# Optimization experiments

Hardware: AMD Instinct MI355X
Metric: run time of the kernel (lower is better)

The kernel has to match this reference:

```python
import jax, jax.numpy as jnp
import numpy as np

N = 50000
E = 400000


def _cheb_norm(edge_index, dtype):
    # PyG ChebConv norm (normalization='sym', lambda_max=2.0):
    # remove self loops, L_hat = -D^{-1/2} A D^{-1/2} on off-diagonal edges.
    src, dst = edge_index[0], edge_index[1]
    mask = (src != dst).astype(dtype)
    deg = jax.ops.segment_sum(mask, src, num_segments=N)
    dinv = jnp.where(deg > 0, jax.lax.rsqrt(jnp.where(deg > 0, deg, 1.0)), 0.0)
    w = -dinv[src] * dinv[dst] * mask  # [E]
    return src, dst, w


def _cheb_conv(x, src, dst, w, W0, W1, b):
    # out = T0(x) W0 + T1(x) W1 + b, T0 = x, T1 = L_hat x
    tx1 = jax.ops.segment_sum(w[:, None] * x[src], dst, num_segments=N)
    return x @ W0 + tx1 @ W1 + b


def setup_inputs() -> dict:
    key = jax.random.key(0)
    ks = jax.random.split(key, 12)
    s = 0.05
    inp = {
        "x": jax.random.normal(ks[0], (N, 128), dtype=jnp.float32),
        "edge_index": jax.random.randint(ks[1], (2, E), 0, N, dtype=jnp.int64),
        "W1_0": jax.random.normal(ks[2], (128, 256), dtype=jnp.float32) * s,
        "W1_1": jax.random.normal(ks[3], (128, 256), dtype=jnp.float32) * s,
        "b1": jnp.zeros((256,), dtype=jnp.float32),
        "W2_0": jax.random.normal(ks[4], (256, 256), dtype=jnp.float32) * s,
        "W2_1": jax.random.normal(ks[5], (256, 256), dtype=jnp.float32) * s,
        "b2": jnp.zeros((256,), dtype=jnp.float32),
        "W3_0": jax.random.normal(ks[6], (256, 256), dtype=jnp.float32) * s,
        "W3_1": jax.random.normal(ks[7], (256, 256), dtype=jnp.float32) * s,
        "b3": jnp.zeros((256,), dtype=jnp.float32),
    }
    return inp


def reference(x, edge_index, W1_0, W1_1, b1, W2_0, W2_1, b2, W3_0, W3_1, b3):
    # Eval mode: F.dropout with training=False is identity, so dropout is omitted.
    src, dst, w = _cheb_norm(edge_index, x.dtype)
    h = jax.nn.relu(_cheb_conv(x, src, dst, w, W1_0, W1_1, b1))
    h = jax.nn.relu(_cheb_conv(h, src, dst, w, W2_0, W2_1, b2))
    h = _cheb_conv(h, src, dst, w, W3_0, W3_1, b3)
    return h
```

## Files before the change

kernel.cpp:

```cpp
#include <hip/hip_runtime.h>
#include <hip/hip_bf16.h>


typedef __attribute__((ext_vector_type(8))) short bf16x8;
typedef __attribute__((ext_vector_type(4))) float f32x4;

__device__ __forceinline__ float bf2f(unsigned int lo16) {
    unsigned int t = lo16 << 16;
    return __builtin_bit_cast(float, t);
}
__device__ __forceinline__ unsigned short f2bf(float f) {
    unsigned int u = __builtin_bit_cast(unsigned int, f);
    unsigned int r = (u + 0x7fffu + ((u >> 16) & 1u)) >> 16;
    return (unsigned short)r;
}

struct PrepParams {
    const int* src;
    const int* dst;
    int* deg;
    int* cnt;
    int* rank;
    int E;
    const float* x;
    unsigned short* xb;
    int gE;
    int gC;
    const float* W[6];
    unsigned short* WT[6];
    int K[6];
};

__global__ __launch_bounds__(256) void prep_kernel(PrepParams p) {
    __shared__ float t[32][33];
    int b = blockIdx.x;
    int tid = threadIdx.x;
    if (b < p.gE) {
        int e = b * 256 + tid;
        if (e < p.E) {
            int s = p.src[e], d = p.dst[e];
            if (s != d) atomicAdd(&p.deg[s], 1);
            p.rank[e] = atomicAdd(&p.cnt[d], 1);
        }
        return;
    }
    b -= p.gE;
    if (b < p.gC) {
        long long i = (long long)b * 256 + tid;
        float4 v = reinterpret_cast<const float4*>(p.x)[i];
        ushort4 o;
        o.x = f2bf(v.x); o.y = f2bf(v.y); o.z = f2bf(v.z); o.w = f2bf(v.w);
        reinterpret_cast<ushort4*>(p.xb)[i] = o;
        return;
    }
    b -= p.gC;
    int m = b >> 6;
    int rem = b & 63;
    int K = p.K[m];
    int kb = (rem & 7) * 32, nb = (rem >> 3) * 32;
    if (kb >= K) return;
    const float* W = p.W[m];
    unsigned short* WT = p.WT[m];
    int lx = tid & 31, ly = tid >> 5;
    #pragma unroll
    for (int i = 0; i < 32; i += 8)
        t[ly + i][lx] = W[(size_t)(kb + ly + i) * 256 + nb + lx];
    __syncthreads();
    #pragma unroll
    for (int i = 0; i < 32; i += 8)
        WT[(size_t)(nb + ly + i) * K + kb + lx] = f2bf(t[lx][ly + i]);
}

__global__ __launch_bounds__(256) void scan_partial_dinv(const int* __restrict__ cnt,
                                                         int* __restrict__ part,
                                                         int* __restrict__ deg, int N) {
    __shared__ int lds[256];
    int tid = threadIdx.x;
    int base = blockIdx.x * 1024 + tid * 4;
    int s = 0;
    #pragma unroll
    for (int i = 0; i < 4; ++i) {
        if (base + i < N) {
            s += cnt[base + i];
            int d = deg[base + i];
            float dv = (d > 0) ? rsqrtf((float)d) : 0.0f;
            reinterpret_cast<float*>(deg)[base + i] = dv;
        }
    }
    lds[tid] = s;
    __syncthreads();
    for (int off = 128; off > 0; off >>= 1) {
        if (tid < off) lds[tid] += lds[tid + off];
        __syncthreads();
    }
    if (tid == 0) part[blockIdx.x] = lds[0];
}

__global__ __launch_bounds__(256) void scan_chunk(const int* __restrict__ cnt,
                                                  const int* __restrict__ part,
                                                  int* __restrict__ rowptr, int N, int NB) {
    __shared__ int lds[256];
    __shared__ int blockOff;
    int tid = threadIdx.x;
    if (tid < 64) {
        int v = (tid < NB) ? part[tid] : 0;
        int inc = v;
        #pragma unroll
        for (int off = 1; off < 64; off <<= 1) {
            int t = __shfl_up(inc, off, 64);
            if (tid >= off) inc += t;
        }
        if (tid == (int)blockIdx.x) blockOff = inc - v;
        if (blockIdx.x == 0 && tid == NB - 1) rowptr[N] = inc;
    }
    __syncthreads();
    int base = blockIdx.x * 1024 + tid * 4;
    int c[4];
    #pragma unroll
    for (int i = 0; i < 4; ++i) c[i] = (base + i < N) ? cnt[base + i] : 0;
    int ts = c[0] + c[1] + c[2] + c[3];
    lds[tid] = ts;
    __syncthreads();
    for (int off = 1; off < 256; off <<= 1) {
        int v = (tid >= off) ? lds[tid - off] : 0;
        __syncthreads();
        lds[tid] += v;
        __syncthreads();
    }
    int o = blockOff + lds[tid] - ts;
    #pragma unroll
    for (int i = 0; i < 4; ++i) {
        if (base + i < N) rowptr[base + i] = o;
        o += c[i];
    }
}

__global__ __launch_bounds__(256) void fill_kernel(const int* __restrict__ src,
                                                   const int* __restrict__ dst,
                                                   const int* __restrict__ rank,
                                                   const float* __restrict__ dinv,
                                                   const int* __restrict__ rowptr,
                                                   int2* __restrict__ epk, int E) {
    int e = blockIdx.x * blockDim.x + threadIdx.x;
    if (e < E) {
        int s = src[e], d = dst[e];
        int pos = rowptr[d] + rank[e];
        float w = (s != d) ? (-dinv[s] * dinv[d]) : 0.0f;
        epk[pos] = make_int2(s, __builtin_bit_cast(int, w));
    }
}

template <int V> struct RowT;
template <> struct RowT<4> { using T = uint2; };
template <> struct RowT<8> { using T = uint4; };

__device__ __forceinline__ void fma_row(float* acc, uint2 u, float wv) {
    acc[0] += wv * bf2f(u.x & 0xffffu);
    acc[1] += wv * bf2f(u.x >> 16);
    acc[2] += wv * bf2f(u.y & 0xffffu);
    acc[3] += wv * bf2f(u.y >> 16);
}
__device__ __forceinline__ void fma_row(float* acc, uint4 u, float wv) {
    acc[0] += wv * bf2f(u.x & 0xffffu);
    acc[1] += wv * bf2f(u.x >> 16);
    acc[2] += wv * bf2f(u.y & 0xffffu);
    acc[3] += wv * bf2f(u.y >> 16);
    acc[4] += wv * bf2f(u.z & 0xffffu);
    acc[5] += wv * bf2f(u.z >> 16);
    acc[6] += wv * bf2f(u.w & 0xffffu);
    acc[7] += wv * bf2f(u.w >> 16);
}
__device__ __forceinline__ void pack_out(unsigned short* q, const float* acc, uint2*) {
    uint2 o;
    o.x = (unsigned int)f2bf(acc[0]) | ((unsigned int)f2bf(acc[1]) << 16);
    o.y = (unsigned int)f2bf(acc[2]) | ((unsigned int)f2bf(acc[3]) << 16);
    *reinterpret_cast<uint2*>(q) = o;
}
__device__ __forceinline__ void pack_out(unsigned short* q, const float* acc, uint4*) {
    uint4 o;
    o.x = (unsigned int)f2bf(acc[0]) | ((unsigned int)f2bf(acc[1]) << 16);
    o.y = (unsigned int)f2bf(acc[2]) | ((unsigned int)f2bf(acc[3]) << 16);
    o.z = (unsigned int)f2bf(acc[4]) | ((unsigned int)f2bf(acc[5]) << 16);
    o.w = (unsigned int)f2bf(acc[6]) | ((unsigned int)f2bf(acc[7]) << 16);
    *reinterpret_cast<uint4*>(q) = o;
}

template <int F>
__global__ __launch_bounds__(256) void gather_bf16(const int* __restrict__ rowptr,
                                                   const int2* __restrict__ epk,
                                                   const unsigned short* __restrict__ xb,
                                                   unsigned short* __restrict__ txb,
                                                   int N) {
    constexpr int V = F / 32;
    using T = typename RowT<V>::T;
    int half = threadIdx.x >> 5;
    int lane = threadIdx.x & 31;
    int n = blockIdx.x * 8 + half;
    if (n >= N) return;
    int beg = rowptr[n], end = rowptr[n + 1];
    float acc[V] = {};

    int k = beg;
    for (; k + 8 <= end; k += 8) {
        int2 ep[8]; T r[8];
        #pragma unroll
        for (int j = 0; j < 8; ++j) ep[j] = epk[k + j];
        #pragma unroll
        for (int j = 0; j < 8; ++j)
            r[j] = *reinterpret_cast<const T*>(&xb[(size_t)ep[j].x * F + lane * V]);
        #pragma unroll
        for (int j = 0; j < 8; ++j)
            fma_row(acc, r[j], __builtin_bit_cast(float, ep[j].y));
    }
    for (; k + 4 <= end; k += 4) {
        int2 e0 = epk[k], e1 = epk[k + 1], e2 = epk[k + 2], e3 = epk[k + 3];
        T r0 = *reinterpret_cast<const T*>(&xb[(size_t)e0.x * F + lane * V]);
        T r1 = *reinterpret_cast<const T*>(&xb[(size_t)e1.x * F + lane * V]);
        T r2 = *reinterpret_cast<const T*>(&xb[(size_t)e2.x * F + lane * V]);
        T r3 = *reinterpret_cast<const T*>(&xb[(size_t)e3.x * F + lane * V]);
        fma_row(acc, r0, __builtin_bit_cast(float, e0.y));
        fma_row(acc, r1, __builtin_bit_cast(float, e1.y));
        fma_row(acc, r2, __builtin_bit_cast(float, e2.y));
        fma_row(acc, r3, __builtin_bit_cast(float, e3.y));
    }
    for (; k < end; ++k) {
        int2 e = epk[k];
        T r = *reinterpret_cast<const T*>(&xb[(size_t)e.x * F + lane * V]);
        fma_row(acc, r, __builtin_bit_cast(float, e.y));
    }

    pack_out(&txb[(size_t)n * F + lane * V], acc, (T*)nullptr);
}

template <int K, bool RELU, typename OutT>
__global__ __launch_bounds__(256, 3) void gemm_mfma(const unsigned short* __restrict__ Xb,
                                                    const unsigned short* __restrict__ Tb,
                                                    const unsigned short* __restrict__ W0T,
                                                    const unsigned short* __restrict__ W1T,
                                                    const float* __restrict__ bias,
                                                    OutT* __restrict__ out, int M) {
    __shared__ unsigned short As[64 * 64];
    __shared__ unsigned short Bs[256 * 64];

    const int tid = threadIdx.x;
    const int wave = tid >> 6;
    const int lane = tid & 63;
    const int l15 = lane & 15;
    const int quad = lane >> 4;
    const int row0 = blockIdx.x * 64;
    const int swz = ((lane & 7) ^ ((lane >> 3) & 7)) * 8;

    f32x4 acc[4][4];
    #pragma unroll
    for (int i = 0; i < 4; ++i)
        #pragma unroll
        for (int j = 0; j < 4; ++j) acc[i][j] = (f32x4){0.f, 0.f, 0.f, 0.f};

    typedef const __attribute__((address_space(1))) void gvoid;
    typedef __attribute__((address_space(3))) void lvoid;

    #pragma unroll
    for (int pass = 0; pass < 2; ++pass) {
        const unsigned short* Amat = pass ? Tb : Xb;
        const unsigned short* Wmat = pass ? W1T : W0T;
        for (int k0 = 0; k0 < K; k0 += 64) {
            if (pass != 0 || k0 != 0) __syncthreads();
            #pragma unroll
            for (int r = 0; r < 2; ++r) {
                int grow = row0 + r * 32 + wave * 8 + (lane >> 3);
                if (grow > M - 1) grow = M - 1;
                const unsigned short* gp = &Amat[(size_t)grow * K + k0 + swz];
                __builtin_amdgcn_global_load_lds((gvoid*)gp,
                    (lvoid*)&As[(r * 32 + wave * 8) * 64], 16, 0, 0);
            }
            #pragma unroll
            for (int r = 0; r < 8; ++r) {
                int brow = r * 32 + wave * 8 + (lane >> 3);
                const unsigned short* gp = &Wmat[(size_t)brow * K + k0 + swz];
                __builtin_amdgcn_global_load_lds((gvoid*)gp,
                    (lvoid*)&Bs[(r * 32 + wave * 8) * 64], 16, 0, 0);
            }
            __syncthreads();

            #pragma unroll
            for (int kf = 0; kf < 2; ++kf) {
                const int col = (((kf * 4 + quad) ^ (l15 & 7)) * 8);
                bf16x8 a[4], b[4];
                #pragma unroll
                for (int mt = 0; mt < 4; ++mt)
                    a[mt] = *reinterpret_cast<const bf16x8*>(&As[(mt * 16 + l15) * 64 + col]);
                #pragma unroll
                for (int nt = 0; nt < 4; ++nt)
                    b[nt] = *reinterpret_cast<const bf16x8*>(
                        &Bs[(wave * 64 + nt * 16 + l15) * 64 + col]);
                #pragma unroll
                for (int mt = 0; mt < 4; ++mt)
                    #pragma unroll
                    for (int nt = 0; nt < 4; ++nt)
                        acc[mt][nt] = __builtin_amdgcn_mfma_f32_16x16x32_bf16(
                            a[mt], b[nt], acc[mt][nt], 0, 0, 0);
            }
        }
    }

    #pragma unroll
    for (int mt = 0; mt < 4; ++mt) {
        #pragma unroll
        for (int r = 0; r < 4; ++r) {
            int m = row0 + mt * 16 + quad * 4 + r;
            if (m >= M) continue;
            #pragma unroll
            for (int nt = 0; nt < 4; ++nt) {
                int n = wave * 64 + nt * 16 + l15;
                float v = acc[mt][nt][r] + bias[n];
                if (RELU) v = fmaxf(v, 0.0f);
                if constexpr (sizeof(OutT) == 2)
                    out[(size_t)m * 256 + n] = (OutT)f2bf(v);
                else
                    out[(size_t)m * 256 + n] = (OutT)v;
            }
        }
    }
}

static inline size_t align_up(size_t v, size_t a) { return (v + a - 1) / a * a; }

extern "C" void kernel_launch(void* const* d_in, const int* in_sizes, int n_in,
                              void* d_out, int out_size, void* d_ws, size_t ws_size,
                              hipStream_t stream) {
    const float* x    = (const float*)d_in[0];
    const int*   ei   = (const int*)d_in[1];
    const float* W1_0 = (const float*)d_in[2];
    const float* W1_1 = (const float*)d_in[3];
    const float* b1   = (const float*)d_in[4];
    const float* W2_0 = (const float*)d_in[5];
    const float* W2_1 = (const float*)d_in[6];
    const float* b2   = (const float*)d_in[7];
    const float* W3_0 = (const float*)d_in[8];
    const float* W3_1 = (const float*)d_in[9];
    const float* b3   = (const float*)d_in[10];
    float* out = (float*)d_out;

    const int N = in_sizes[0] / 128;
    const int E = in_sizes[1] / 2;
    const int* src = ei;
    const int* dst = ei + E;

    typedef unsigned short u16;
    char* ws = (char*)d_ws;
    size_t off = 0;
    int*   deg    = (int*)  (ws + off); off = align_up(off + (size_t)N * 4, 256);
    int*   cnt    = (int*)  (ws + off); off = align_up(off + (size_t)N * 4, 256);
    size_t zero_end = off;
    int*   rank   = (int*)  (ws + off); off = align_up(off + (size_t)E * 4, 256);
    int*   rowptr = (int*)  (ws + off); off = align_up(off + (size_t)(N + 1) * 4, 256);
    int*   part   = (int*)  (ws + off); off = align_up(off + 256 * 4, 256);
    int2*  epk    = (int2*) (ws + off); off = align_up(off + (size_t)E * 8, 256);
    u16*   xb     = (u16*)  (ws + off); off = align_up(off + (size_t)N * 128 * 2, 256);
    u16*   txb    = (u16*)  (ws + off); off = align_up(off + (size_t)N * 256 * 2, 256);
    u16*   h1b    = (u16*)  (ws + off); off = align_up(off + (size_t)N * 256 * 2, 256);
    u16*   h2b    = (u16*)  (ws + off); off = align_up(off + (size_t)N * 256 * 2, 256);
    u16*   W10T   = (u16*)  (ws + off); off = align_up(off + (size_t)256 * 128 * 2, 256);
    u16*   W11T   = (u16*)  (ws + off); off = align_up(off + (size_t)256 * 128 * 2, 256);
    u16*   W20T   = (u16*)  (ws + off); off = align_up(off + (size_t)256 * 256 * 2, 256);
    u16*   W21T   = (u16*)  (ws + off); off = align_up(off + (size_t)256 * 256 * 2, 256);
    u16*   W30T   = (u16*)  (ws + off); off = align_up(off + (size_t)256 * 256 * 2, 256);
    u16*   W31T   = (u16*)  (ws + off); off = align_up(off + (size_t)256 * 256 * 2, 256);
    (void)ws_size;

    const int TB = 256;
    const int gE = (E + TB - 1) / TB;
    const int gC = (int)(((long long)N * 128 / 4) / 256);
    const int NB = (N + 1023) / 1024;

    hipMemsetAsync(deg, 0, zero_end, stream);

    {
        PrepParams p;
        p.src = src; p.dst = dst; p.deg = deg; p.cnt = cnt; p.rank = rank; p.E = E;
        p.x = x; p.xb = xb; p.gE = gE; p.gC = gC;
        p.W[0] = W1_0; p.WT[0] = W10T; p.K[0] = 128;
        p.W[1] = W1_1; p.WT[1] = W11T; p.K[1] = 128;
        p.W[2] = W2_0; p.WT[2] = W20T; p.K[2] = 256;
        p.W[3] = W2_1; p.WT[3] = W21T; p.K[3] = 256;
        p.W[4] = W3_0; p.WT[4] = W30T; p.K[4] = 256;
        p.W[5] = W3_1; p.WT[5] = W31T; p.K[5] = 256;
        prep_kernel<<<gE + gC + 384, TB, 0, stream>>>(p);
    }

    scan_partial_dinv<<<NB, 256, 0, stream>>>(cnt, part, deg, N);
    scan_chunk<<<NB, 256, 0, stream>>>(cnt, part, rowptr, N, NB);
    fill_kernel<<<(E + TB - 1) / TB, TB, 0, stream>>>(src, dst, rank,
                                                      (const float*)deg, rowptr, epk, E);

    dim3 gemmGrid((N + 63) / 64);
    dim3 gatherGrid((N + 7) / 8);

    gather_bf16<128><<<gatherGrid, TB, 0, stream>>>(rowptr, epk, xb, txb, N);
    gemm_mfma<128, true, u16><<<gemmGrid, TB, 0, stream>>>(xb, txb, W10T, W11T, b1, h1b, N);

    gather_bf16<256><<<gatherGrid, TB, 0, stream>>>(rowptr, epk, h1b, txb, N);
    gemm_mfma<256, true, u16><<<gemmGrid, TB, 0, stream>>>(h1b, txb, W20T, W21T, b2, h2b, N);

    gather_bf16<256><<<gatherGrid, TB, 0, stream>>>(rowptr, epk, h2b, txb, N);
    gemm_mfma<256, false, float><<<gemmGrid, TB, 0, stream>>>(h2b, txb, W30T, W31T, b3, out, N);
}
```

Baseline: 315.1 us.

## Double-buffer GEMM LDS tiles to overlap global loads with MFMA

The fused two-pass ChebConv GEMM now runs as a single loop over K-steps with ping-pong shared-memory buffers. Each step prefetches the next A/W tile with global_load_lds while it computes MFMAs on the current tile, and uses one barrier per step instead of two. It also raises wave priority around the MFMA block. The price is double the LDS per block (about 80KB), so launch bounds drop from 3 blocks per CU to 2, which lowers occupancy.

```diff
diff --git a/kernel.cpp b/kernel.cpp
--- a/kernel.cpp
+++ b/kernel.cpp
@@ -233,14 +233,16 @@
 }
 
 template <int K, bool RELU, typename OutT>
-__global__ __launch_bounds__(256, 3) void gemm_mfma(const unsigned short* __restrict__ Xb,
+__global__ __launch_bounds__(256, 2) void gemm_mfma(const unsigned short* __restrict__ Xb,
                                                     const unsigned short* __restrict__ Tb,
                                                     const unsigned short* __restrict__ W0T,
                                                     const unsigned short* __restrict__ W1T,
                                                     const float* __restrict__ bias,
                                                     OutT* __restrict__ out, int M) {
-    __shared__ unsigned short As[64 * 64];
-    __shared__ unsigned short Bs[256 * 64];
+    constexpr int KSTEPS = K / 64;
+    constexpr int NT = 2 * KSTEPS;
+    __shared__ unsigned short As[2][64 * 64];
+    __shared__ unsigned short Bs[2][256 * 64];
 
     const int tid = threadIdx.x;
     const int wave = tid >> 6;
@@ -259,48 +261,55 @@
     typedef const __attribute__((address_space(1))) void gvoid;
     typedef __attribute__((address_space(3))) void lvoid;
 
-    #pragma unroll
-    for (int pass = 0; pass < 2; ++pass) {
-        const unsigned short* Amat = pass ? Tb : Xb;
-        const unsigned short* Wmat = pass ? W1T : W0T;
-        for (int k0 = 0; k0 < K; k0 += 64) {
-            if (pass != 0 || k0 != 0) __syncthreads();
+    auto stage = [&](int t, int buf) {
+        const unsigned short* Amat = (t < KSTEPS) ? Xb : Tb;
+        const unsigned short* Wmat = (t < KSTEPS) ? W0T : W1T;
+        const int k0 = (t & (KSTEPS - 1)) * 64;
+        #pragma unroll
+        for (int r = 0; r < 2; ++r) {
+            int grow = row0 + r * 32 + wave * 8 + (lane >> 3);
+            if (grow > M - 1) grow = M - 1;
+            const unsigned short* gp = &Amat[(size_t)grow * K + k0 + swz];
+            __builtin_amdgcn_global_load_lds((gvoid*)gp,
+                (lvoid*)&As[buf][(r * 32 + wave * 8) * 64], 16, 0, 0);
+        }
+        #pragma unroll
+        for (int r = 0; r < 8; ++r) {
+            int brow = r * 32 + wave * 8 + (lane >> 3);
+            const unsigned short* gp = &Wmat[(size_t)brow * K + k0 + swz];
+            __builtin_amdgcn_global_load_lds((gvoid*)gp,
+                (lvoid*)&Bs[buf][(r * 32 + wave * 8) * 64], 16, 0, 0);
+        }
+    };
+
+    stage(0, 0);
+    __syncthreads();
+
+    int cur = 0;
+    for (int t = 0; t < NT; ++t) {
+        if (t + 1 < NT) stage(t + 1, cur ^ 1);
+        #pragma unroll
+        for (int kf = 0; kf < 2; ++kf) {
+            const int col = (((kf * 4 + quad) ^ (l15 & 7)) * 8);
+            bf16x8 a[4], b[4];
             #pragma unroll
-            for (int r = 0; r < 2; ++r) {
-                int grow = row0 + r * 32 + wave * 8 + (lane >> 3);
-                if (grow > M - 1) grow = M - 1;
-                const unsigned short* gp = &Amat[(size_t)grow * K + k0 + swz];
-                __builtin_amdgcn_global_load_lds((gvoid*)gp,
-                    (lvoid*)&As[(r * 32 + wave * 8) * 64], 16, 0, 0);
-            }
+            for (int mt = 0; mt < 4; ++mt)
+                a[mt] = *reinterpret_cast<const bf16x8*>(&As[cur][(mt * 16 + l15) * 64 + col]);
             #pragma unroll
-            for (int r = 0; r < 8; ++r) {
-                int brow = r * 32 + wave * 8 + (lane >> 3);
-                const unsigned short* gp = &Wmat[(size_t)brow * K + k0 + swz];
-                __builtin_amdgcn_global_load_lds((gvoid*)gp,
-                    (lvoid*)&Bs[(r * 32 + wave * 8) * 64], 16, 0, 0);
-            }
-            __syncthreads();
-
+            for (int nt = 0; nt < 4; ++nt)
+                b[nt] = *reinterpret_cast<const bf16x8*>(
+                    &Bs[cur][(wave * 64 + nt * 16 + l15) * 64 + col]);
+            __builtin_amdgcn_s_setprio(1);
             #pragma unroll
-            for (int kf = 0; kf < 2; ++kf) {
-                const int col = (((kf * 4 + quad) ^ (l15 & 7)) * 8);
-                bf16x8 a[4], b[4];
-                #pragma unroll
-                for (int mt = 0; mt < 4; ++mt)
-                    a[mt] = *reinterpret_cast<const bf16x8*>(&As[(mt * 16 + l15) * 64 + col]);
+            for (int mt = 0; mt < 4; ++mt)
                 #pragma unroll
                 for (int nt = 0; nt < 4; ++nt)
-                    b[nt] = *reinterpret_cast<const bf16x8*>(
-                        &Bs[(wave * 64 + nt * 16 + l15) * 64 + col]);
-                #pragma unroll
-                for (int mt = 0; mt < 4; ++mt)
-                    #pragma unroll
-                    for (int nt = 0; nt < 4; ++nt)
-                        acc[mt][nt] = __builtin_amdgcn_mfma_f32_16x16x32_bf16(
-                            a[mt], b[nt], acc[mt][nt], 0, 0, 0);
-            }
-        }
+                    acc[mt][nt] = __builtin_amdgcn_mfma_f32_16x16x32_bf16(
+                        a[mt], b[nt], acc[mt][nt], 0, 0, 0);
+            __builtin_amdgcn_s_setprio(0);
+        }
+        __syncthreads();
+        cur ^= 1;
     }
 
     #pragma unroll
```

After: 320.8 us. About the same (+1.8%).
